# Kernel optimization log

Hardware: AMD Instinct MI355X
Metric: run time of the kernel (lower is better)

The kernel has to match this reference:

```python
import jax, jax.numpy as jnp
import numpy as np

B, L = 4, 2048
D_MODEL, D_INNER, D_STATE, DT_RANK, K = 512, 1024, 16, 64, 4


def setup_inputs() -> dict:
    key = jax.random.key(0)
    ks = jax.random.split(key, 21)
    def n(k, shape, s=0.02):
        return (jax.random.normal(k, shape) * s).astype(jnp.float32)
    inp = {"x": jax.random.normal(ks[0], (B, L, D_MODEL), jnp.float32)}
    for i, sfx in enumerate(("f", "b")):
        o = 1 + i * 8
        inp[f"W_in_{sfx}"] = n(ks[o], (2 * D_INNER, D_MODEL))
        inp[f"conv_w_{sfx}"] = n(ks[o + 1], (D_INNER, 1, K), 0.1)
        inp[f"conv_b_{sfx}"] = jnp.zeros((D_INNER,), jnp.float32)
        inp[f"A_log_{sfx}"] = (jax.random.normal(ks[o + 2], (D_STATE, D_INNER)) * 0.1).astype(jnp.float32)
        inp[f"D_{sfx}"] = jnp.ones((D_INNER,), jnp.float32)
        inp[f"Wx_{sfx}"] = n(ks[o + 3], (DT_RANK + 2 * D_STATE, D_INNER))
        inp[f"Wdt_{sfx}"] = n(ks[o + 4], (D_INNER, DT_RANK), DT_RANK ** -0.5)
        dt = jnp.exp(jax.random.uniform(ks[o + 5], (D_INNER,)) * (np.log(0.1) - np.log(0.001)) + np.log(0.001))
        inp[f"bdt_{sfx}"] = (dt + jnp.log(-jnp.expm1(-dt))).astype(jnp.float32)
        inp[f"Wout_{sfx}"] = n(ks[o + 6], (D_MODEL, D_INNER))
    return inp


def _mamba_block(x, W_in, conv_w, conv_b, A_log, Dp, Wx, Wdt, bdt, Wout):
    # x: [B, L, d_model]
    xz = jnp.einsum('bld,ed->ble', x, W_in)              # [B, L, 2*d_inner]
    xb, zb = xz[..., :D_INNER], xz[..., D_INNER:]
    # causal depthwise conv over time
    xc = jnp.transpose(xb, (0, 2, 1))                     # [B, M, L]
    xc = jax.lax.conv_general_dilated(
        xc, conv_w, window_strides=(1,), padding=[(K - 1, 0)],
        feature_group_count=D_INNER,
        dimension_numbers=('NCH', 'OIH', 'NCH')) + conv_b[None, :, None]
    xb = jax.nn.silu(jnp.transpose(xc, (0, 2, 1)))        # [B, L, M]
    # input-dependent SSM parameters
    proj = jnp.einsum('blm,pm->blp', xb, Wx)              # [B, L, dt_rank+2D]
    dt_in = proj[..., :DT_RANK]
    Bs = proj[..., DT_RANK:DT_RANK + D_STATE]             # [B, L, D]
    Cs = proj[..., DT_RANK + D_STATE:]                    # [B, L, D]
    dt = jax.nn.softplus(jnp.einsum('blr,mr->blm', dt_in, Wdt) + bdt)  # [B, L, M]
    A_T = -jnp.exp(A_log).T                               # [M, D]

    def step(h, inp):
        dt_t, x_t, B_t, C_t = inp                         # [B,M],[B,M],[B,D],[B,D]
        dA = jnp.exp(dt_t[:, :, None] * A_T[None])        # [B, M, D]
        h = dA * h + (dt_t * x_t)[:, :, None] * B_t[:, None, :]
        y_t = jnp.einsum('bmd,bd->bm', h, C_t)
        return h, y_t

    xs = (jnp.moveaxis(dt, 1, 0), jnp.moveaxis(xb, 1, 0),
          jnp.moveaxis(Bs, 1, 0), jnp.moveaxis(Cs, 1, 0))
    h0 = jnp.zeros((x.shape[0], D_INNER, D_STATE), x.dtype)
    _, ys = jax.lax.scan(step, h0, xs)                    # [L, B, M]
    y = jnp.moveaxis(ys, 0, 1) + Dp * xb                  # [B, L, M]
    y = y * jax.nn.silu(zb)                               # SiLU gate
    return jnp.einsum('blm,dm->bld', y, Wout)             # [B, L, d_model]


def reference(x,
              W_in_f, conv_w_f, conv_b_f, A_log_f, D_f, Wx_f, Wdt_f, bdt_f, Wout_f,
              W_in_b, conv_w_b, conv_b_b, A_log_b, D_b, Wx_b, Wdt_b, bdt_b, Wout_b):
    out_f = _mamba_block(x, W_in_f, conv_w_f, conv_b_f, A_log_f, D_f, Wx_f, Wdt_f, bdt_f, Wout_f)
    out_b = jnp.flip(_mamba_block(jnp.flip(x, 1), W_in_b, conv_w_b, conv_b_b, A_log_b, D_b, Wx_b, Wdt_b, bdt_b, Wout_b), 1)
    return out_f + out_b
```

## Files before the change

### kernel.cpp

```cpp
#include <hip/hip_runtime.h>
#include <hip/hip_bf16.h>
#include <cstdint>
#include <cstdio>

typedef float f32x4 __attribute__((ext_vector_type(4)));
typedef short s16x8 __attribute__((ext_vector_type(8)));
typedef unsigned int u32x2 __attribute__((ext_vector_type(2)));

__device__ __forceinline__ float us2f(unsigned short u){
  union { unsigned int i; float f; } v; v.i = ((unsigned int)u) << 16; return v.f;
}
__device__ __forceinline__ unsigned short f2us(float f){
  union { float f; unsigned int i; } v; v.f = f;
  unsigned int r = v.i + 0x7fffu + ((v.i >> 16) & 1u);
  return (unsigned short)(r >> 16);
}
__device__ __forceinline__ void gload_lds16(const void* g, void* l){
  __builtin_amdgcn_global_load_lds(
      (const __attribute__((address_space(1))) unsigned int*)g,
      (__attribute__((address_space(3))) unsigned int*)l, 16, 0, 0);
}

#define PK0 0.999962f


__global__ __launch_bounds__(256)
void prep_k(const float* __restrict__ x,
            const float* __restrict__ W_in_f, const float* __restrict__ W_in_b,
            const float* __restrict__ Wx_f,   const float* __restrict__ Wx_b,
            const float* __restrict__ Wdt_f,  const float* __restrict__ Wdt_b,
            const float* __restrict__ Wout_f, const float* __restrict__ Wout_b,
            const float* __restrict__ Alog_f, const float* __restrict__ Alog_b,
            const float* __restrict__ bdt_f,  const float* __restrict__ bdt_b,
            unsigned short* __restrict__ W1p, unsigned short* __restrict__ Wxp,
            unsigned short* __restrict__ Wdtp,  unsigned short* __restrict__ Woutp,
            float* __restrict__ A2, float* __restrict__ bdtcat,
            unsigned short* __restrict__ xbf, float* __restrict__ Cf)
{
  long i = (long)blockIdx.x * 256 + threadIdx.x;
  if (i < 4194304) {
    xbf[i] = f2us(x[i]); return;
  }
  i -= 4194304;
  if (i < 2097152) {
    int n = (int)(i >> 9), k = (int)(i & 511);
    float v = (n < 2048) ? W_in_f[(long)n*512 + k] : W_in_b[(long)(n-2048)*512 + k];
    W1p[((long)(k >> 3)*4096 + n)*8 + (k & 7)] = f2us(v); return;
  }
  i -= 2097152;
  if (i < 262144) {
    int dir = (int)(i >> 17); long r = i & 131071; int n = (int)(r >> 10), k = (int)(r & 1023);
    const float* Wx = dir ? Wx_b : Wx_f;
    Wxp[(long)dir*131072 + ((long)(k >> 3)*128 + n)*8 + (k & 7)] =
        f2us(n < 96 ? Wx[(long)n*1024 + k] : 0.f);
    return;
  }
  i -= 262144;
  if (i < 131072) {
    int dir = (int)(i >> 16); long r = i & 65535; int n = (int)(r >> 6), k = (int)(r & 63);
    Wdtp[(long)dir*65536 + ((long)(k >> 3)*1024 + n)*8 + (k & 7)] =
        f2us((dir ? Wdt_b : Wdt_f)[r]);
    return;
  }
  i -= 131072;
  if (i < 1048576) {
    int n = (int)(i >> 11), k = (int)(i & 2047);
    float v = (k < 1024) ? Wout_f[(long)n*1024 + k] : Wout_b[(long)n*1024 + (k-1024)];
    Woutp[((long)(k >> 3)*512 + n)*8 + (k & 7)] = f2us(v); return;
  }
  i -= 1048576;
  if (i < 32768) {
    int dir = (int)(i >> 14); long r = i & 16383; int m = (int)(r >> 4), d = (int)(r & 15);
    const float* Al = dir ? Alog_b : Alog_f;
    A2[i] = -__expf(Al[(long)d*1024 + m]) * 1.4426950408889634f; return;
  }
  i -= 32768;
  if (i < 2048) {
    int dir = (int)(i >> 10), m = (int)(i & 1023);
    bdtcat[i] = (dir ? bdt_b : bdt_f)[m]; return;
  }
  i -= 2048;
  if (i < 98304) {
    int dir = (int)(i / 49152); long r = i % 49152;
    int m = (int)(r / 48), j = (int)(r % 48);
    int k = j >> 4, d = j & 15;
    const float* Al = dir ? Alog_b : Alog_f;
    const float w = -__expf(Al[(long)d*1024 + m]);
    float c;
    if (k == 0)      c = 0.999150f * w;
    else if (k == 1) c = 0.492809f * w * w;
    else             c = 0.139212f * w * w * w;
    Cf[(long)dir*49152 + (long)m*48 + (k << 4) + d] = c;
    return;
  }
}

template<int OUT_MODE, int DBUF>
__global__ __launch_bounds__(256)
void gemm_bt(const unsigned short* __restrict__ Ap, const unsigned short* __restrict__ Bp,
             void* __restrict__ Cp, const float* __restrict__ biasp,
             float* __restrict__ bcf,
             int K, int lda, int ldb, int ldc,
             long az, long bz, long cz, int biasz)
{
  const int z   = blockIdx.z;
  const int tid = threadIdx.x;
  const int bm  = blockIdx.x, bn = blockIdx.y;

  __shared__ __align__(16) unsigned short Ash[1+DBUF][128][64];

  const int wave = tid >> 6, lane = tid & 63;
  const int wr = (wave >> 1) << 6, wc = (wave & 1) << 6;
  const int fr = lane & 15, fs = lane >> 4;

  const int rr  = tid >> 3;
  const int csp = tid & 7;
  const int csg = ((csp ^ (rr & 7)) << 3);

  const unsigned short* Ag = Ap + (long)z * az;
  const unsigned short* Bg = Bp + (long)z * bz;

  const long abase = (long)(bm*128 + rr)*lda + csg;
  const unsigned short* Bt = Bg + ((long)fs*ldb + bn*128 + wc + fr)*8;

  f32x4 acc[4][4];
  #pragma unroll
  for (int i=0;i<4;i++)
    #pragma unroll
    for (int j=0;j<4;j++) acc[i][j] = (f32x4){0.f,0.f,0.f,0.f};

  const int NK = K >> 6;

  auto stage = [&](int buf, int ks){
    const long k0 = (long)ks << 6;
    #pragma unroll
    for (int r=0;r<4;r++)
      gload_lds16(Ag + abase + (long)(r*32)*lda + k0, &Ash[buf][rr + r*32][csp << 3]);
  };
  auto compute = [&](int buf, int ks){
    #pragma unroll
    for (int sub=0; sub<2; ++sub){
      const unsigned short* Bk = Bt + (long)(ks*8 + sub*4)*ldb*8;
      s16x8 af[4], bfv[4];
      #pragma unroll
      for (int j=0;j<4;j++) bfv[j] = *(const s16x8*)(Bk + j*128);
      #pragma unroll
      for (int i=0;i<4;i++){
        const int ar = wr + i*16 + fr;
        af[i] = *(const s16x8*)&Ash[buf][ar][(((sub<<2)+fs) ^ (fr&7)) << 3];
      }
      #pragma unroll
      for (int i=0;i<4;i++)
        #pragma unroll
        for (int j=0;j<4;j++)
          acc[i][j] = __builtin_amdgcn_mfma_f32_16x16x32_bf16(bfv[j], af[i], acc[i][j], 0, 0, 0);
    }
  };

  if (DBUF){
    stage(0, 0);
    int cur = 0;
    for (int ks = 0; ks < NK; ++ks){
      __syncthreads();
      if (ks + 1 < NK) stage(cur ^ 1, ks + 1);
      compute(cur, ks);
      cur ^= 1;
    }
  } else {
    for (int ks = 0; ks < NK; ++ks){
      __syncthreads();
      stage(0, ks);
      __syncthreads();
      compute(0, ks);
    }
  }

  #pragma unroll
  for (int i=0;i<4;i++){
    const int row = bm*128 + wr + i*16 + fr;
    #pragma unroll
    for (int j=0;j<4;j++){
      const int c0 = bn*128 + wc + j*16 + (fs << 2);
      f32x4 v = acc[i][j];
      const long cbase = (long)z*cz + (long)row*ldc + c0;
      if (OUT_MODE == 2){
        *(f32x4*)((float*)Cp + cbase) = v;
      } else if (OUT_MODE == 1){
        const f32x4 b4 = *(const f32x4*)(biasp + z*biasz + c0);
        u32x2 o;
        unsigned short s[4];
        #pragma unroll
        for (int e=0;e<4;e++){
          float t = v[e] + b4[e];
          t = fmaxf(t, 0.f) + log1pf(__expf(-fabsf(t)));
          s[e] = f2us(t);
        }
        o[0] = (unsigned int)s[0] | ((unsigned int)s[1] << 16);
        o[1] = (unsigned int)s[2] | ((unsigned int)s[3] << 16);
        *(u32x2*)((unsigned short*)Cp + cbase) = o;
      } else {
        if (OUT_MODE == 4 && ((c0 >> 10) & 1)){
          #pragma unroll
          for (int e=0;e<4;e++) v[e] = v[e] / (1.f + __expf(-v[e]));
        }
        u32x2 o;
        o[0] = (unsigned int)f2us(v[0]) | ((unsigned int)f2us(v[1]) << 16);
        o[1] = (unsigned int)f2us(v[2]) | ((unsigned int)f2us(v[3]) << 16);
        *(u32x2*)((unsigned short*)Cp + cbase) = o;
        if (OUT_MODE == 3 && c0 >= 64 && c0 < 96){
          *(f32x4*)(bcf + ((long)z*8192 + row)*32 + (c0 - 64)) = v;
        }
      }
    }
  }
}

__global__ __launch_bounds__(256)
void conv_silu_k(const unsigned short* __restrict__ xz,
                 const float* __restrict__ wf, const float* __restrict__ cbf,
                 const float* __restrict__ wb, const float* __restrict__ cbb,
                 unsigned short* __restrict__ xbc)
{
  const int tid = threadIdx.x;
  const long tok = blockIdx.x;
  const int l   = (int)(tok & 2047);
  const int dir = tid >> 7;
  const int mg  = (tid & 127) << 3;
  const float* w  = dir ? wb  : wf;
  const float* cb = dir ? cbb : cbf;
  const long rowb = tok << 12;
  const int  xcol = (dir << 11) + mg;

  f32x4 wv[8];
  #pragma unroll
  for (int e=0;e<8;e++) wv[e] = *(const f32x4*)(w + (mg + e)*4);
  const f32x4 cb0 = *(const f32x4*)(cb + mg);
  const f32x4 cb1 = *(const f32x4*)(cb + mg + 4);

  float acc[8];
  #pragma unroll
  for (int e=0;e<4;e++){ acc[e]=cb0[e]; acc[4+e]=cb1[e]; }

  #pragma unroll
  for (int k=0;k<4;k++){
    const int off = dir ? (3 - k) : (k - 3);
    const int pos = l + off;
    if (pos >= 0 && pos < 2048){
      const s16x8 xv = *(const s16x8*)(xz + rowb + ((long)off << 12) + xcol);
      #pragma unroll
      for (int e=0;e<8;e++)
        acc[e] = __builtin_fmaf(wv[e][k], us2f((unsigned short)xv[e]), acc[e]);
    }
  }
  s16x8 out;
  #pragma unroll
  for (int e=0;e<8;e++){
    const float s = acc[e] / (1.f + __expf(-acc[e]));
    out[e] = (short)f2us(s);
  }
  *(s16x8*)(xbc + tok*2048 + (dir << 10) + mg) = out;
}

#define SCHUNK 32
#define NCHUNK 64

__global__ __launch_bounds__(256)
void scan1_k(const unsigned short* __restrict__ dtb, const unsigned short* __restrict__ xbc,
             const float* __restrict__ BCf, const float* __restrict__ Cf,
             unsigned short* __restrict__ hloc, float* __restrict__ Ssum)
{
  const int tidx = threadIdx.x;
  const int cb = blockIdx.x, c = blockIdx.y, bz = blockIdx.z;
  const int b = bz >> 1, dir = bz & 1;
  const int m = cb*256 + tidx;

  float C1[16], C2[16], C3[16];
  { const f32x4* p = (const f32x4*)(Cf + ((long)dir*1024 + m)*48);
    #pragma unroll
    for (int q=0;q<4;q++){
      f32x4 v1=p[q], v2=p[q+4], v3=p[q+8];
      #pragma unroll
      for (int e=0;e<4;e++){ C1[q*4+e]=v1[e]; C2[q*4+e]=v2[e]; C3[q*4+e]=v3[e]; } } }

  const int  l0 = dir ? (2047 - c*SCHUNK) : (c*SCHUNK);
  const int  ls = dir ? -1 : 1;
  const long tok0 = (long)b*2048 + l0;

  __shared__ float Bs[SCHUNK][16];
  if (tidx < 128){
    const int r = tidx >> 2, c4 = (tidx & 3) << 2;
    *(f32x4*)&Bs[r][c4] =
        *(const f32x4*)(BCf + ((long)dir*8192 + tok0 + (long)ls*r)*32 + c4);
  }
  __syncthreads();

  const unsigned short* dtp = dtb + ((long)dir << 23) + tok0*1024 + m;
  const unsigned short* xvp = xbc + tok0*2048 + (dir << 10) + m;
  const long dstp = (long)ls*1024, xstp = (long)ls*2048;

  float h[16];
  #pragma unroll
  for (int d=0;d<16;d++) h[d]=0.f;
  float S = 0.f;

  unsigned short du = *dtp, xu = *xvp;
  for (int t=0;t<SCHUNK;t++){
    const float dt = us2f(du), xv = us2f(xu);
    dtp += dstp; xvp += xstp;
    du = *dtp; xu = *xvp;
    S += dt;
    const float u = dt * xv;
    const float dt2 = dt*dt, dt3 = dt2*dt;
    const f32x4 bv0 = *(const f32x4*)&Bs[t][0];
    const f32x4 bv1 = *(const f32x4*)&Bs[t][4];
    const f32x4 bv2 = *(const f32x4*)&Bs[t][8];
    const f32x4 bv3 = *(const f32x4*)&Bs[t][12];
    #pragma unroll
    for (int d=0;d<16;d++){
      const float bval = (d<4)? bv0[d&3] : (d<8)? bv1[d&3] : (d<12)? bv2[d&3] : bv3[d&3];
      float a = __builtin_fmaf(C1[d], dt, PK0);
      a = __builtin_fmaf(C2[d], dt2, a);
      a = __builtin_fmaf(C3[d], dt3, a);
      h[d] = __builtin_fmaf(a, h[d], u * bval);
    }
  }
  const long o = (((long)bz * NCHUNK) + c)*1024 + m;
  s16x8 hv0, hv1;
  #pragma unroll
  for (int e=0;e<8;e++){ hv0[e] = (short)f2us(h[e]); hv1[e] = (short)f2us(h[8+e]); }
  *(s16x8*)(hloc + (o << 4))     = hv0;
  *(s16x8*)(hloc + (o << 4) + 8) = hv1;
  Ssum[o] = S;
}

__global__ __launch_bounds__(256)
void scan2_k(const float* __restrict__ A2, const float* __restrict__ Ssum,
             unsigned short* __restrict__ hloc)
{
  const long idx = (long)blockIdx.x*256 + threadIdx.x;
  const long bz = idx >> 14; const int r = (int)(idx & 16383);
  const int dir = (int)(bz & 1);
  const float a2 = A2[((long)dir << 14) + r];
  const long base = bz * NCHUNK;
  float hs = 0.f;
  float hlN = us2f(hloc[base*16384 + r]);
  float SN  = Ssum[base*1024 + (r >> 4)];
  for (int c=0;c<NCHUNK;c++){
    const float hl = hlN, Sv = SN;
    const int cn = (c+1 < NCHUNK) ? c+1 : c;
    hlN = us2f(hloc[(base+cn)*16384 + r]);
    SN  = Ssum[(base+cn)*1024 + (r >> 4)];
    const float P = __builtin_amdgcn_exp2f(a2 * Sv);
    hloc[(base+c)*16384 + r] = f2us(hs);
    hs = __builtin_fmaf(P, hs, hl);
  }
}

__global__ __launch_bounds__(256)
void scan3_k(const unsigned short* __restrict__ dtb, const unsigned short* __restrict__ xbc,
             const float* __restrict__ BCf, const float* __restrict__ Cf,
             const unsigned short* __restrict__ hstart, const unsigned short* __restrict__ xz,
             const float* __restrict__ D_f, const float* __restrict__ D_b,
             unsigned short* __restrict__ ybuf)
{
  const int tidx = threadIdx.x;
  const int cb = blockIdx.x, c = blockIdx.y, bz = blockIdx.z;
  const int b = bz >> 1, dir = bz & 1;
  const int m = cb*256 + tidx;

  float C1[16], C2[16], C3[16];
  { const f32x4* p = (const f32x4*)(Cf + ((long)dir*1024 + m)*48);
    #pragma unroll
    for (int q=0;q<4;q++){
      f32x4 v1=p[q], v2=p[q+4], v3=p[q+8];
      #pragma unroll
      for (int e=0;e<4;e++){ C1[q*4+e]=v1[e]; C2[q*4+e]=v2[e]; C3[q*4+e]=v3[e]; } } }
  const float Dm = (dir ? D_b : D_f)[m];

  const int  l0 = dir ? (2047 - c*SCHUNK) : (c*SCHUNK);
  const int  ls = dir ? -1 : 1;
  const long tok0 = (long)b*2048 + l0;

  __shared__ float BC[SCHUNK][32];
  { const int r = tidx >> 3, c4 = (tidx & 7) << 2;
    *(f32x4*)&BC[r][c4] =
        *(const f32x4*)(BCf + ((long)dir*8192 + tok0 + (long)ls*r)*32 + c4); }

  float h[16];
  { const long o = ((((long)bz*NCHUNK) + c)*1024 + m) << 4;
    s16x8 hv0 = *(const s16x8*)(hstart + o);
    s16x8 hv1 = *(const s16x8*)(hstart + o + 8);
    #pragma unroll
    for (int e=0;e<8;e++){ h[e] = us2f((unsigned short)hv0[e]);
                           h[8+e] = us2f((unsigned short)hv1[e]); } }
  __syncthreads();

  const unsigned short* dtp = dtb + ((long)dir << 23) + tok0*1024 + m;
  const unsigned short* xvp = xbc + tok0*2048 + (dir << 10) + m;
  const unsigned short* zp  = xz  + (tok0 << 12) + (dir << 11) + 1024 + m;
  unsigned short*       yp  = ybuf + tok0*2048 + (dir << 10) + m;
  const long dstp = (long)ls*1024, xstp = (long)ls*2048, zstp = (long)ls << 12;

  unsigned short du = *dtp, xu = *xvp, zu = *zp;
  for (int t=0;t<SCHUNK;t++){
    const float dt = us2f(du), xv = us2f(xu), gate = us2f(zu);
    dtp += dstp; xvp += xstp; zp += zstp;
    du = *dtp; xu = *xvp; zu = *zp;
    const float u = dt * xv;
    const float dt2 = dt*dt, dt3 = dt2*dt;
    const f32x4 bv0 = *(const f32x4*)&BC[t][0];
    const f32x4 bv1 = *(const f32x4*)&BC[t][4];
    const f32x4 bv2 = *(const f32x4*)&BC[t][8];
    const f32x4 bv3 = *(const f32x4*)&BC[t][12];
    const f32x4 cv0 = *(const f32x4*)&BC[t][16];
    const f32x4 cv1 = *(const f32x4*)&BC[t][20];
    const f32x4 cv2 = *(const f32x4*)&BC[t][24];
    const f32x4 cv3 = *(const f32x4*)&BC[t][28];
    float y0=0.f, y1=0.f;
    #pragma unroll
    for (int d=0;d<16;d++){
      const float bval = (d<4)? bv0[d&3] : (d<8)? bv1[d&3] : (d<12)? bv2[d&3] : bv3[d&3];
      const float cval = (d<4)? cv0[d&3] : (d<8)? cv1[d&3] : (d<12)? cv2[d&3] : cv3[d&3];
      float a = __builtin_fmaf(C1[d], dt, PK0);
      a = __builtin_fmaf(C2[d], dt2, a);
      a = __builtin_fmaf(C3[d], dt3, a);
      h[d] = __builtin_fmaf(a, h[d], u * bval);
      if (d & 1) y1 = __builtin_fmaf(h[d], cval, y1);
      else       y0 = __builtin_fmaf(h[d], cval, y0);
    }
    const float y = (y0 + y1) + Dm * xv;
    *yp = f2us(y * gate);
    yp += xstp;
  }
}

extern "C" void kernel_launch(void* const* d_in, const int* in_sizes, int n_in,
                              void* d_out, int out_size, void* d_ws, size_t ws_size,
                              hipStream_t stream)
{
  const float* x      = (const float*)d_in[0];
  const float* W_in_f = (const float*)d_in[1];
  const float* convw_f= (const float*)d_in[2];
  const float* convb_f= (const float*)d_in[3];
  const float* Alog_f = (const float*)d_in[4];
  const float* D_f    = (const float*)d_in[5];
  const float* Wx_f   = (const float*)d_in[6];
  const float* Wdt_f  = (const float*)d_in[7];
  const float* bdt_f  = (const float*)d_in[8];
  const float* Wout_f = (const float*)d_in[9];
  const float* W_in_b = (const float*)d_in[10];
  const float* convw_b= (const float*)d_in[11];
  const float* convb_b= (const float*)d_in[12];
  const float* Alog_b = (const float*)d_in[13];
  const float* D_b    = (const float*)d_in[14];
  const float* Wx_b   = (const float*)d_in[15];
  const float* Wdt_b  = (const float*)d_in[16];
  const float* bdt_b  = (const float*)d_in[17];
  const float* Wout_b = (const float*)d_in[18];

  char* w = (char*)d_ws;
  auto carve = [&](size_t bytes) -> char* {
    char* p = w; w += (bytes + 255) & ~(size_t)255; return p;
  };
  unsigned short* W1p     = (unsigned short*)carve(4096ULL*512*2);
  unsigned short* Wxp     = (unsigned short*)carve(2ULL*128*1024*2);
  unsigned short* Wdtp    = (unsigned short*)carve(2ULL*1024*64*2);
  unsigned short* Woutp   = (unsigned short*)carve(512ULL*2048*2);
  float*          A2      = (float*)carve(2ULL*1024*16*4);
  float*          bdtcat  = (float*)carve(2048ULL*4);
  float*          Cf      = (float*)carve(2ULL*1024*48*4);
  float*          BCf     = (float*)carve(2ULL*8192*32*4);
  unsigned short* xz      = (unsigned short*)carve(8192ULL*4096*2);
  unsigned short* xbc     = (unsigned short*)carve(8192ULL*2048*2);
  unsigned short* proj    = (unsigned short*)carve(2ULL*8192*128*2);
  unsigned short* dtb     = (unsigned short*)carve(2ULL*8192*1024*2);
  unsigned short* ybuf    = (unsigned short*)carve(8192ULL*2048*2);
  unsigned short* hloc    = (unsigned short*)carve(8ULL*NCHUNK*1024*16*2);
  float*          Ssum    = (float*)carve(8ULL*NCHUNK*1024*4);
  unsigned short* xbf     = ybuf;

  if ((size_t)(w - (char*)d_ws) > ws_size) {
    fprintf(stderr, "kernel_launch: ws too small (%zu needed, %zu given)\n",
            (size_t)(w - (char*)d_ws), ws_size);
    return;
  }

  prep_k<<<dim3(30728), 256, 0, stream>>>(x, W_in_f, W_in_b, Wx_f, Wx_b, Wdt_f, Wdt_b,
                                          Wout_f, Wout_b, Alog_f, Alog_b, bdt_f, bdt_b,
                                          W1p, Wxp, Wdtp, Woutp, A2, bdtcat, xbf, Cf);
  gemm_bt<4,1><<<dim3(64,32,1), 256, 0, stream>>>(xbf, W1p, xz, nullptr, nullptr,
                                                  512, 512, 4096, 4096, 0, 0, 0, 0);
  conv_silu_k<<<dim3(8192), 256, 0, stream>>>(xz, convw_f, convb_f, convw_b, convb_b, xbc);
  gemm_bt<3,1><<<dim3(64,1,2), 256, 0, stream>>>(xbc, Wxp, proj, nullptr, BCf,
                                                 1024, 2048, 128, 128,
                                                 1024, 131072, 1048576, 0);
  gemm_bt<1,0><<<dim3(64,8,2), 256, 0, stream>>>(proj, Wdtp, dtb, bdtcat, nullptr,
                                                 64, 128, 1024, 1024,
                                                 1048576, 65536, 8388608, 1024);
  scan1_k<<<dim3(4,NCHUNK,8), 256, 0, stream>>>(dtb, xbc, BCf, Cf, hloc, Ssum);
  scan2_k<<<dim3(512), 256, 0, stream>>>(A2, Ssum, hloc);
  scan3_k<<<dim3(4,NCHUNK,8), 256, 0, stream>>>(dtb, xbc, BCf, Cf, hloc, xz, D_f, D_b, ybuf);
  gemm_bt<2,1><<<dim3(64,4,1), 256, 0, stream>>>(ybuf, Woutp, d_out, nullptr, nullptr,
                                                 2048, 2048, 512, 512, 0, 0, 0, 0);
}
```

Measured before the change: 332.2 us.

## Prefetch GEMM B-fragments into registers and pack scan recurrences as float2 FMAs

The GEMM main loop is unrolled by two with ping-pong LDS buffers, and the global B-fragment loads for the next k-step are issued into registers before the current step's MFMAs, so their latency overlaps compute. All GEMM instantiations now use double buffering, including the small K=64 one. The scan1 and scan3 inner loops are rewritten on float2 vectors so the compiler can emit packed FMA instructions, aiming to halve the VALU instruction count of the recurrence. The cost is higher register pressure from holding 16 extra B fragments, which could lower occupancy.

```diff
diff --git a/kernel.cpp b/kernel.cpp
--- a/kernel.cpp
+++ b/kernel.cpp
@@ -4,6 +4,7 @@
 #include <cstdio>
 
 typedef float f32x4 __attribute__((ext_vector_type(4)));
+typedef float f32x2 __attribute__((ext_vector_type(2)));
 typedef short s16x8 __attribute__((ext_vector_type(8)));
 typedef unsigned int u32x2 __attribute__((ext_vector_type(2)));
 
@@ -95,7 +96,7 @@
   }
 }
 
-template<int OUT_MODE, int DBUF>
+template<int OUT_MODE>
 __global__ __launch_bounds__(256)
 void gemm_bt(const unsigned short* __restrict__ Ap, const unsigned short* __restrict__ Bp,
              void* __restrict__ Cp, const float* __restrict__ biasp,
@@ -107,7 +108,7 @@
   const int tid = threadIdx.x;
   const int bm  = blockIdx.x, bn = blockIdx.y;
 
-  __shared__ __align__(16) unsigned short Ash[1+DBUF][128][64];
+  __shared__ __align__(16) unsigned short Ash[2][128][64];
 
   const int wave = tid >> 6, lane = tid & 63;
   const int wr = (wave >> 1) << 6, wc = (wave & 1) << 6;
@@ -137,13 +138,18 @@
     for (int r=0;r<4;r++)
       gload_lds16(Ag + abase + (long)(r*32)*lda + k0, &Ash[buf][rr + r*32][csp << 3]);
   };
-  auto compute = [&](int buf, int ks){
+  auto loadB = [&](int ks, s16x8* bf){
     #pragma unroll
     for (int sub=0; sub<2; ++sub){
       const unsigned short* Bk = Bt + (long)(ks*8 + sub*4)*ldb*8;
-      s16x8 af[4], bfv[4];
       #pragma unroll
-      for (int j=0;j<4;j++) bfv[j] = *(const s16x8*)(Bk + j*128);
+      for (int j=0;j<4;j++) bf[sub*4+j] = *(const s16x8*)(Bk + j*128);
+    }
+  };
+  auto compute = [&](int buf, const s16x8* bf){
+    #pragma unroll
+    for (int sub=0; sub<2; ++sub){
+      s16x8 af[4];
       #pragma unroll
       for (int i=0;i<4;i++){
         const int ar = wr + i*16 + fr;
@@ -153,26 +159,21 @@
       for (int i=0;i<4;i++)
         #pragma unroll
         for (int j=0;j<4;j++)
-          acc[i][j] = __builtin_amdgcn_mfma_f32_16x16x32_bf16(bfv[j], af[i], acc[i][j], 0, 0, 0);
+          acc[i][j] = __builtin_amdgcn_mfma_f32_16x16x32_bf16(bf[sub*4+j], af[i], acc[i][j], 0, 0, 0);
     }
   };
 
-  if (DBUF){
-    stage(0, 0);
-    int cur = 0;
-    for (int ks = 0; ks < NK; ++ks){
-      __syncthreads();
-      if (ks + 1 < NK) stage(cur ^ 1, ks + 1);
-      compute(cur, ks);
-      cur ^= 1;
-    }
-  } else {
-    for (int ks = 0; ks < NK; ++ks){
-      __syncthreads();
-      stage(0, ks);
-      __syncthreads();
-      compute(0, ks);
-    }
+  s16x8 bA[8], bB[8];
+  stage(0, 0);
+  loadB(0, bA);
+  for (int ks = 0; ks < NK; ks += 2){
+    __syncthreads();
+    if (ks + 1 < NK){ stage(1, ks + 1); loadB(ks + 1, bB); }
+    compute(0, bA);
+    if (ks + 1 >= NK) break;
+    __syncthreads();
+    if (ks + 2 < NK){ stage(0, ks + 2); loadB(ks + 2, bA); }
+    compute(1, bB);
   }
 
   #pragma unroll
@@ -274,13 +275,16 @@
   const int b = bz >> 1, dir = bz & 1;
   const int m = cb*256 + tidx;
 
-  float C1[16], C2[16], C3[16];
+  f32x2 C1v[8], C2v[8], C3v[8];
   { const f32x4* p = (const f32x4*)(Cf + ((long)dir*1024 + m)*48);
     #pragma unroll
     for (int q=0;q<4;q++){
       f32x4 v1=p[q], v2=p[q+4], v3=p[q+8];
-      #pragma unroll
-      for (int e=0;e<4;e++){ C1[q*4+e]=v1[e]; C2[q*4+e]=v2[e]; C3[q*4+e]=v3[e]; } } }
+      C1v[2*q]   = (f32x2){v1[0], v1[1]};  C1v[2*q+1] = (f32x2){v1[2], v1[3]};
+      C2v[2*q]   = (f32x2){v2[0], v2[1]};  C2v[2*q+1] = (f32x2){v2[2], v2[3]};
+      C3v[2*q]   = (f32x2){v3[0], v3[1]};  C3v[2*q+1] = (f32x2){v3[2], v3[3]};
+    } }
+  const f32x2 k0v = {PK0, PK0};
 
   const int  l0 = dir ? (2047 - c*SCHUNK) : (c*SCHUNK);
   const int  ls = dir ? -1 : 1;
@@ -298,9 +302,9 @@
   const unsigned short* xvp = xbc + tok0*2048 + (dir << 10) + m;
   const long dstp = (long)ls*1024, xstp = (long)ls*2048;
 
-  float h[16];
-  #pragma unroll
-  for (int d=0;d<16;d++) h[d]=0.f;
+  f32x2 h2[8];
+  #pragma unroll
+  for (int p=0;p<8;p++) h2[p] = (f32x2){0.f, 0.f};
   float S = 0.f;
 
   unsigned short du = *dtp, xu = *xvp;
@@ -311,23 +315,23 @@
     S += dt;
     const float u = dt * xv;
     const float dt2 = dt*dt, dt3 = dt2*dt;
-    const f32x4 bv0 = *(const f32x4*)&Bs[t][0];
-    const f32x4 bv1 = *(const f32x4*)&Bs[t][4];
-    const f32x4 bv2 = *(const f32x4*)&Bs[t][8];
-    const f32x4 bv3 = *(const f32x4*)&Bs[t][12];
-    #pragma unroll
-    for (int d=0;d<16;d++){
-      const float bval = (d<4)? bv0[d&3] : (d<8)? bv1[d&3] : (d<12)? bv2[d&3] : bv3[d&3];
-      float a = __builtin_fmaf(C1[d], dt, PK0);
-      a = __builtin_fmaf(C2[d], dt2, a);
-      a = __builtin_fmaf(C3[d], dt3, a);
-      h[d] = __builtin_fmaf(a, h[d], u * bval);
+    const f32x2 dtv = {dt, dt}, dt2v = {dt2, dt2}, dt3v = {dt3, dt3}, uv = {u, u};
+    const f32x2* b2 = (const f32x2*)&Bs[t][0];
+    #pragma unroll
+    for (int p=0;p<8;p++){
+      f32x2 a = __builtin_elementwise_fma(C1v[p], dtv, k0v);
+      a = __builtin_elementwise_fma(C2v[p], dt2v, a);
+      a = __builtin_elementwise_fma(C3v[p], dt3v, a);
+      h2[p] = __builtin_elementwise_fma(a, h2[p], uv * b2[p]);
     }
   }
   const long o = (((long)bz * NCHUNK) + c)*1024 + m;
   s16x8 hv0, hv1;
   #pragma unroll
-  for (int e=0;e<8;e++){ hv0[e] = (short)f2us(h[e]); hv1[e] = (short)f2us(h[8+e]); }
+  for (int e=0;e<4;e++){
+    hv0[2*e]   = (short)f2us(h2[e][0]);     hv0[2*e+1] = (short)f2us(h2[e][1]);
+    hv1[2*e]   = (short)f2us(h2[4+e][0]);   hv1[2*e+1] = (short)f2us(h2[4+e][1]);
+  }
   *(s16x8*)(hloc + (o << 4))     = hv0;
   *(s16x8*)(hloc + (o << 4) + 8) = hv1;
   Ssum[o] = S;
@@ -368,13 +372,16 @@
   const int b = bz >> 1, dir = bz & 1;
   const int m = cb*256 + tidx;
 
-  float C1[16], C2[16], C3[16];
+  f32x2 C1v[8], C2v[8], C3v[8];
   { const f32x4* p = (const f32x4*)(Cf + ((long)dir*1024 + m)*48);
     #pragma unroll
     for (int q=0;q<4;q++){
       f32x4 v1=p[q], v2=p[q+4], v3=p[q+8];
-      #pragma unroll
-      for (int e=0;e<4;e++){ C1[q*4+e]=v1[e]; C2[q*4+e]=v2[e]; C3[q*4+e]=v3[e]; } } }
+      C1v[2*q]   = (f32x2){v1[0], v1[1]};  C1v[2*q+1] = (f32x2){v1[2], v1[3]};
+      C2v[2*q]   = (f32x2){v2[0], v2[1]};  C2v[2*q+1] = (f32x2){v2[2], v2[3]};
+      C3v[2*q]   = (f32x2){v3[0], v3[1]};  C3v[2*q+1] = (f32x2){v3[2], v3[3]};
+    } }
+  const f32x2 k0v = {PK0, PK0};
   const float Dm = (dir ? D_b : D_f)[m];
 
   const int  l0 = dir ? (2047 - c*SCHUNK) : (c*SCHUNK);
@@ -386,13 +393,15 @@
     *(f32x4*)&BC[r][c4] =
         *(const f32x4*)(BCf + ((long)dir*8192 + tok0 + (long)ls*r)*32 + c4); }
 
-  float h[16];
+  f32x2 h2[8];
   { const long o = ((((long)bz*NCHUNK) + c)*1024 + m) << 4;
     s16x8 hv0 = *(const s16x8*)(hstart + o);
     s16x8 hv1 = *(const s16x8*)(hstart + o + 8);
     #pragma unroll
-    for (int e=0;e<8;e++){ h[e] = us2f((unsigned short)hv0[e]);
-                           h[8+e] = us2f((unsigned short)hv1[e]); } }
+    for (int e=0;e<4;e++){
+      h2[e]   = (f32x2){us2f((unsigned short)hv0[2*e]), us2f((unsigned short)hv0[2*e+1])};
+      h2[4+e] = (f32x2){us2f((unsigned short)hv1[2*e]), us2f((unsigned short)hv1[2*e+1])};
+    } }
   __syncthreads();
 
   const unsigned short* dtp = dtb + ((long)dir << 23) + tok0*1024 + m;
@@ -408,27 +417,19 @@
     du = *dtp; xu = *xvp; zu = *zp;
     const float u = dt * xv;
     const float dt2 = dt*dt, dt3 = dt2*dt;
-    const f32x4 bv0 = *(const f32x4*)&BC[t][0];
-    const f32x4 bv1 = *(const f32x4*)&BC[t][4];
-    const f32x4 bv2 = *(const f32x4*)&BC[t][8];
-    const f32x4 bv3 = *(const f32x4*)&BC[t][12];
-    const f32x4 cv0 = *(const f32x4*)&BC[t][16];
-    const f32x4 cv1 = *(const f32x4*)&BC[t][20];
-    const f32x4 cv2 = *(const f32x4*)&BC[t][24];
-    const f32x4 cv3 = *(const f32x4*)&BC[t][28];
-    float y0=0.f, y1=0.f;
-    #pragma unroll
-    for (int d=0;d<16;d++){
-      const float bval = (d<4)? bv0[d&3] : (d<8)? bv1[d&3] : (d<12)? bv2[d&3] : bv3[d&3];
-      const float cval = (d<4)? cv0[d&3] : (d<8)? cv1[d&3] : (d<12)? cv2[d&3] : cv3[d&3];
-      float a = __builtin_fmaf(C1[d], dt, PK0);
-      a = __builtin_fmaf(C2[d], dt2, a);
-      a = __builtin_fmaf(C3[d], dt3, a);
-      h[d] = __builtin_fmaf(a, h[d], u * bval);
-      if (d & 1) y1 = __builtin_fmaf(h[d], cval, y1);
-      else       y0 = __builtin_fmaf(h[d], cval, y0);
+    const f32x2 dtv = {dt, dt}, dt2v = {dt2, dt2}, dt3v = {dt3, dt3}, uv = {u, u};
+    const f32x2* bc2 = (const f32x2*)&BC[t][0];
+    f32x2 y2a = {0.f, 0.f}, y2b = {0.f, 0.f};
+    #pragma unroll
+    for (int p=0;p<8;p++){
+      f32x2 a = __builtin_elementwise_fma(C1v[p], dtv, k0v);
+      a = __builtin_elementwise_fma(C2v[p], dt2v, a);
+      a = __builtin_elementwise_fma(C3v[p], dt3v, a);
+      h2[p] = __builtin_elementwise_fma(a, h2[p], uv * bc2[p]);
+      if (p & 1) y2b = __builtin_elementwise_fma(h2[p], bc2[8+p], y2b);
+      else       y2a = __builtin_elementwise_fma(h2[p], bc2[8+p], y2a);
     }
-    const float y = (y0 + y1) + Dm * xv;
+    const float y = ((y2a[0] + y2a[1]) + (y2b[0] + y2b[1])) + Dm * xv;
     *yp = f2us(y * gate);
     yp += xstp;
   }
@@ -488,18 +489,18 @@
   prep_k<<<dim3(30728), 256, 0, stream>>>(x, W_in_f, W_in_b, Wx_f, Wx_b, Wdt_f, Wdt_b,
                                           Wout_f, Wout_b, Alog_f, Alog_b, bdt_f, bdt_b,
                                           W1p, Wxp, Wdtp, Woutp, A2, bdtcat, xbf, Cf);
-  gemm_bt<4,1><<<dim3(64,32,1), 256, 0, stream>>>(xbf, W1p, xz, nullptr, nullptr,
-                                                  512, 512, 4096, 4096, 0, 0, 0, 0);
+  gemm_bt<4><<<dim3(64,32,1), 256, 0, stream>>>(xbf, W1p, xz, nullptr, nullptr,
+                                                512, 512, 4096, 4096, 0, 0, 0, 0);
   conv_silu_k<<<dim3(8192), 256, 0, stream>>>(xz, convw_f, convb_f, convw_b, convb_b, xbc);
-  gemm_bt<3,1><<<dim3(64,1,2), 256, 0, stream>>>(xbc, Wxp, proj, nullptr, BCf,
-                                                 1024, 2048, 128, 128,
-                                                 1024, 131072, 1048576, 0);
-  gemm_bt<1,0><<<dim3(64,8,2), 256, 0, stream>>>(proj, Wdtp, dtb, bdtcat, nullptr,
-                                                 64, 128, 1024, 1024,
-                                                 1048576, 65536, 8388608, 1024);
+  gemm_bt<3><<<dim3(64,1,2), 256, 0, stream>>>(xbc, Wxp, proj, nullptr, BCf,
+                                               1024, 2048, 128, 128,
+                                               1024, 131072, 1048576, 0);
+  gemm_bt<1><<<dim3(64,8,2), 256, 0, stream>>>(proj, Wdtp, dtb, bdtcat, nullptr,
+                                               64, 128, 1024, 1024,
+                                               1048576, 65536, 8388608, 1024);
   scan1_k<<<dim3(4,NCHUNK,8), 256, 0, stream>>>(dtb, xbc, BCf, Cf, hloc, Ssum);
   scan2_k<<<dim3(512), 256, 0, stream>>>(A2, Ssum, hloc);
   scan3_k<<<dim3(4,NCHUNK,8), 256, 0, stream>>>(dtb, xbc, BCf, Cf, hloc, xz, D_f, D_b, ybuf);
-  gemm_bt<2,1><<<dim3(64,4,1), 256, 0, stream>>>(ybuf, Woutp, d_out, nullptr, nullptr,
-                                                 2048, 2048, 512, 512, 0, 0, 0, 0);
-}
+  gemm_bt<2><<<dim3(64,4,1), 256, 0, stream>>>(ybuf, Woutp, d_out, nullptr, nullptr,
+                                               2048, 2048, 512, 512, 0, 0, 0, 0);
+}
```

Result: slower. 345.2 us (+3.9%).
